# Performance work log

Measured on AMD Instinct MI355X. Metric: run time of the kernel, lower is better.

The kernel has to match this reference:

```python
import jax, jax.numpy as jnp
import numpy as np

N_CODEBOOKS = 4
CODEBOOK_SIZE = 1024
CODEBOOK_DIM = 8
INPUT_DIM = 512
EPS_NORM = 1e-12  # F.normalize eps
EPS_SCALE = 1e-8


def _normalize(x, eps=EPS_NORM):
    n = jnp.linalg.norm(x, axis=-1, keepdims=True)
    return x / jnp.maximum(n, eps)


def _wn_weight(v, g):
    # weight-norm 1x1 conv weight: v [out, in], g [out]
    return g[:, None] * v / jnp.maximum(jnp.linalg.norm(v, axis=1, keepdims=True), EPS_NORM)


def _vq_step(residual, v_in, g_in, b_in, v_out, g_out, b_out, cb):
    # residual: [B, D, T]
    sg = jax.lax.stop_gradient
    w_in = _wn_weight(v_in, g_in)                                   # [cd, D]
    z_e = jnp.einsum('od,bdt->bot', w_in, residual) + b_in[None, :, None]  # [B, cd, T]

    # nearest-code search on L2-normalized vectors (same argmin as the cdist form)
    enc = jnp.transpose(z_e, (0, 2, 1))                             # [B, T, cd]
    sim = jnp.einsum('btd,kd->btk', _normalize(enc), _normalize(cb))
    idx = jnp.argmax(sim, axis=-1)                                  # [B, T]
    q_tok = cb[idx]                                                 # [B, T, cd]
    z_q_pre = jnp.transpose(q_tok, (0, 2, 1))                       # [B, cd, T]

    commit = jnp.mean((z_e - sg(z_q_pre)) ** 2, axis=(1, 2))        # [B]
    codeb = jnp.mean((z_q_pre - sg(z_e)) ** 2, axis=(1, 2))         # [B]

    # rotation trick: z_q = scale * (I - 2 r r^T + 2 q_n e_n^T) z_e, R/scale stop-grad
    e = enc                                                         # [B, T, cd]
    e_n = sg(_normalize(e))
    q_n = sg(_normalize(q_tok))
    r = sg(_normalize(e_n + q_n))
    scale = sg(jnp.linalg.norm(q_tok, axis=-1, keepdims=True)
               / jnp.maximum(jnp.linalg.norm(e, axis=-1, keepdims=True), EPS_SCALE))
    re = jnp.sum(r * e, axis=-1, keepdims=True)
    ene = jnp.sum(e_n * e, axis=-1, keepdims=True)
    z_rot = scale * (e - 2.0 * r * re + 2.0 * q_n * ene)            # [B, T, cd]
    z_q = jnp.transpose(z_rot, (0, 2, 1))                           # [B, cd, T]

    w_out = _wn_weight(v_out, g_out)                                # [D, cd]
    z_q_i = jnp.einsum('od,bdt->bot', w_out, z_q) + b_out[None, :, None]  # [B, D, T]
    return z_q_i, commit, codeb, idx


def setup_inputs() -> dict:
    key = jax.random.key(0)
    ks = jax.random.split(key, 8)
    B, D, T = 16, INPUT_DIM, 4096
    nq, K, cd = N_CODEBOOKS, CODEBOOK_SIZE, CODEBOOK_DIM
    return {
        'z': jax.random.normal(ks[0], (B, D, T), dtype=jnp.float32),
        'in_proj_v': jax.random.normal(ks[1], (nq, cd, D), dtype=jnp.float32) * (1.0 / np.sqrt(D)),
        'in_proj_g': jnp.ones((nq, cd), dtype=jnp.float32),
        'in_proj_b': jnp.zeros((nq, cd), dtype=jnp.float32),
        'out_proj_v': jax.random.normal(ks[2], (nq, D, cd), dtype=jnp.float32) * (1.0 / np.sqrt(cd)),
        'out_proj_g': jnp.ones((nq, D), dtype=jnp.float32),
        'out_proj_b': jnp.zeros((nq, D), dtype=jnp.float32),
        'codebooks': jax.random.normal(ks[3], (nq, K, cd), dtype=jnp.float32),
    }


def reference(z, in_proj_v, in_proj_g, in_proj_b, out_proj_v, out_proj_g, out_proj_b, codebooks):
    # eval-mode RVQ forward: all N_CODEBOOKS codebooks active (mask all ones)
    z_q = jnp.zeros_like(z)
    residual = z
    commitment_loss = jnp.float32(0.0)
    codebook_loss = jnp.float32(0.0)
    codes = []
    for i in range(N_CODEBOOKS):
        z_q_i, commit_i, codeb_i, idx_i = _vq_step(
            residual, in_proj_v[i], in_proj_g[i], in_proj_b[i],
            out_proj_v[i], out_proj_g[i], out_proj_b[i], codebooks[i])
        z_q = z_q + z_q_i
        residual = residual - z_q_i
        commitment_loss = commitment_loss + jnp.mean(commit_i)
        codebook_loss = codebook_loss + jnp.mean(codeb_i)
        codes.append(idx_i)
    return z_q, jnp.stack(codes, axis=0), commitment_loss, codebook_loss
```

## Files before the change

### kernel.cpp

```cpp
#include <hip/hip_runtime.h>
#include <cstddef>

#define NQ 4
#define KCODES 1024
#define CD 8
#define DIM 512
#define BATCH 16
#define TLEN 4096
#define TT 32
#define NTHREADS 512

#define WS_WIN  0
#define WS_WOUT (NQ * DIM * CD)
#define WS_CBN  (2 * NQ * DIM * CD)
#define OUT_ZQ 0
#define OUT_CODES ((size_t)BATCH * DIM * TLEN)
#define OUT_LOSS (OUT_CODES + (size_t)NQ * BATCH * TLEN)

__global__ void rvq_zero(float* out) {
  out[OUT_LOSS] = 0.f;
  out[OUT_LOSS + 1] = 0.f;
}

__global__ void rvq_prep(const float* __restrict__ inv, const float* __restrict__ ing,
                         const float* __restrict__ outv, const float* __restrict__ outg,
                         const float* __restrict__ cb, float* __restrict__ ws) {
  const int blk = blockIdx.x, tid = threadIdx.x;
  if (blk < 32) {
    const int i = blk >> 3, o = blk & 7;
    const float* v = inv + (size_t)(i * CD + o) * DIM;
    const float a = v[tid], b = v[tid + 256];
    float s = a * a + b * b;
    #pragma unroll
    for (int off = 32; off >= 1; off >>= 1) s += __shfl_xor(s, off);
    __shared__ float red[4];
    if ((tid & 63) == 0) red[tid >> 6] = s;
    __syncthreads();
    const float nrm = fmaxf(sqrtf(red[0] + red[1] + red[2] + red[3]), 1e-12f);
    const float g = ing[i * CD + o];
    ws[WS_WIN + (size_t)((i * DIM + tid) * CD) + o] = (g * a) / nrm;
    ws[WS_WIN + (size_t)((i * DIM + tid + 256) * CD) + o] = (g * b) / nrm;
  } else {
    const int rid = (blk - 32) * 256 + tid;
    if (rid < NQ * DIM) {
      const float* v = outv + (size_t)rid * CD;
      float vv[8]; float n2 = 0.f;
      #pragma unroll
      for (int o = 0; o < 8; ++o) { vv[o] = v[o]; n2 += vv[o] * vv[o]; }
      const float nrm = fmaxf(sqrtf(n2), 1e-12f);
      const float g = outg[rid];
      #pragma unroll
      for (int o = 0; o < 8; ++o) ws[WS_WOUT + (size_t)rid * CD + o] = (g * vv[o]) / nrm;
    } else {
      const int k = rid - NQ * DIM;
      const float* v = cb + (size_t)k * CD;
      float vv[8]; float n2 = 0.f;
      #pragma unroll
      for (int o = 0; o < 8; ++o) { vv[o] = v[o]; n2 += vv[o] * vv[o]; }
      const float nrm = fmaxf(sqrtf(n2), 1e-12f);
      #pragma unroll
      for (int o = 0; o < 8; ++o) ws[WS_CBN + (size_t)k * CD + o] = vv[o] / nrm;
    }
  }
}

__launch_bounds__(NTHREADS, 4)
__global__ void rvq_main(const float* __restrict__ z,
                         const float* __restrict__ b_in, const float* __restrict__ b_out,
                         const float* __restrict__ cb, const float* __restrict__ ws,
                         float* __restrict__ out) {
  extern __shared__ float lds[];
  float* res  = lds;
  float* part = lds + DIM * TT;
  float* ze   = part + 8 * TT * 9;
  float* sc   = ze + TT * 9;
  int*   idl  = (int*)(sc + 16 * TT);

  const int tid = threadIdx.x;
  const int bb = blockIdx.x >> 7;
  const int t0 = (blockIdx.x & 127) * TT;

  const float* zb = z + (size_t)bb * DIM * TLEN + t0;

  {
    const int q = tid & 7, d0 = tid >> 3;
    #pragma unroll
    for (int p = 0; p < 8; ++p) {
      const int d = d0 + p * 64;
      const float4 v = *(const float4*)(zb + (size_t)d * TLEN + q * 4);
      *(float4*)(res + d * TT + q * 4) = v;
    }
  }
  __syncthreads();

  const int t  = tid & 31;
  const int dc = tid >> 5;
  const int w  = tid >> 6;
  float loss_acc = 0.f;

  for (int i = 0; i < NQ; ++i) {
    float acc[8] = {0,0,0,0,0,0,0,0};
    {
      const float* wp = ws + WS_WIN + (size_t)(i * DIM + dc * 32) * CD;
      const float* rp = res + dc * 32 * TT + t;
      #pragma unroll 4
      for (int j = 0; j < 32; ++j) {
        const float r = rp[j * TT];
        const float4 w0 = *(const float4*)(wp + j * 8);
        const float4 w1 = *(const float4*)(wp + j * 8 + 4);
        acc[0] += w0.x * r; acc[1] += w0.y * r; acc[2] += w0.z * r; acc[3] += w0.w * r;
        acc[4] += w1.x * r; acc[5] += w1.y * r; acc[6] += w1.z * r; acc[7] += w1.w * r;
      }
    }
    #pragma unroll
    for (int o = 0; o < 8; ++o) acc[o] += __shfl_xor(acc[o], 32);
    if ((tid & 63) < 32) {
      float* pp = part + (w * TT + t) * 9;
      #pragma unroll
      for (int o = 0; o < 8; ++o) pp[o] = acc[o];
    }
    __syncthreads();
    if (tid < 256) {
      const int tt2 = tid >> 3, o = tid & 7;
      float s = b_in[i * CD + o];
      #pragma unroll
      for (int ww = 0; ww < 8; ++ww) s += part[(ww * TT + tt2) * 9 + o];
      ze[tt2 * 9 + o] = s;
    }
    __syncthreads();

    float e[8], en[8];
    #pragma unroll
    for (int o = 0; o < 8; ++o) e[o] = ze[t * 9 + o];
    float ne2 = 0.f;
    #pragma unroll
    for (int o = 0; o < 8; ++o) ne2 += e[o] * e[o];
    const float ne = sqrtf(ne2);
    const float ned = fmaxf(ne, 1e-12f);
    #pragma unroll
    for (int o = 0; o < 8; ++o) en[o] = e[o] / ned;

    float best = -1e30f; int bk = 0;
    {
      const float* cp = ws + WS_CBN + (size_t)(i * KCODES + dc * 64) * CD;
      #pragma unroll 4
      for (int k = 0; k < 64; ++k) {
        const float4 c0 = *(const float4*)(cp + k * 8);
        const float4 c1 = *(const float4*)(cp + k * 8 + 4);
        const float s = en[0]*c0.x + en[1]*c0.y + en[2]*c0.z + en[3]*c0.w
                      + en[4]*c1.x + en[5]*c1.y + en[6]*c1.z + en[7]*c1.w;
        if (s > best) { best = s; bk = dc * 64 + k; }
      }
    }
    sc[tid] = best;
    idl[tid] = bk;
    __syncthreads();
    best = -1e30f; bk = KCODES;
    #pragma unroll
    for (int cc = 0; cc < 16; ++cc) {
      const float s2 = sc[cc * TT + t];
      const int k2 = idl[cc * TT + t];
      if (s2 > best || (s2 == best && k2 < bk)) { best = s2; bk = k2; }
    }
    if (tid < TT) {
      out[OUT_CODES + (size_t)(i * BATCH + bb) * TLEN + t0 + tid] = (float)bk;
    }

    float qv[8];
    {
      const float* qp = cb + (size_t)(i * KCODES + bk) * CD;
      const float4 q0 = *(const float4*)qp;
      const float4 q1 = *(const float4*)(qp + 4);
      qv[0]=q0.x; qv[1]=q0.y; qv[2]=q0.z; qv[3]=q0.w;
      qv[4]=q1.x; qv[5]=q1.y; qv[6]=q1.z; qv[7]=q1.w;
    }
    if (tid < TT) {
      float s = 0.f;
      #pragma unroll
      for (int o = 0; o < 8; ++o) { const float d2 = e[o] - qv[o]; s += d2 * d2; }
      loss_acc += s;
    }
    float nq2 = 0.f;
    #pragma unroll
    for (int o = 0; o < 8; ++o) nq2 += qv[o] * qv[o];
    const float nq = sqrtf(nq2);
    const float nqd = fmaxf(nq, 1e-12f);
    float qn[8], ru[8];
    float nr2 = 0.f;
    #pragma unroll
    for (int o = 0; o < 8; ++o) { qn[o] = qv[o] / nqd; ru[o] = en[o] + qn[o]; nr2 += ru[o] * ru[o]; }
    const float nrd = fmaxf(sqrtf(nr2), 1e-12f);
    const float scale = nq / fmaxf(ne, 1e-8f);
    float re = 0.f, ene = 0.f;
    #pragma unroll
    for (int o = 0; o < 8; ++o) { ru[o] = ru[o] / nrd; re += ru[o] * e[o]; ene += en[o] * e[o]; }
    float zr[8];
    #pragma unroll
    for (int o = 0; o < 8; ++o) zr[o] = scale * (e[o] - 2.f * ru[o] * re + 2.f * qn[o] * ene);

    {
      const float* wp2 = ws + WS_WOUT + (size_t)(i * DIM + dc * 32) * CD;
      const float* bp2 = b_out + i * DIM + dc * 32;
      float* rp2 = res + dc * 32 * TT + t;
      #pragma unroll 4
      for (int j = 0; j < 32; ++j) {
        const float4 w0 = *(const float4*)(wp2 + j * 8);
        const float4 w1 = *(const float4*)(wp2 + j * 8 + 4);
        float v = bp2[j];
        v += w0.x*zr[0] + w0.y*zr[1] + w0.z*zr[2] + w0.w*zr[3]
           + w1.x*zr[4] + w1.y*zr[5] + w1.z*zr[6] + w1.w*zr[7];
        rp2[j * TT] -= v;
      }
    }
    __syncthreads();
  }

  {
    const int q = tid & 7, d0 = tid >> 3;
    float* ob = out + OUT_ZQ + (size_t)bb * DIM * TLEN + t0;
    #pragma unroll
    for (int p = 0; p < 8; ++p) {
      const int d = d0 + p * 64;
      const float4 v = *(const float4*)(zb + (size_t)d * TLEN + q * 4);
      const float4 r4 = *(const float4*)(res + d * TT + q * 4);
      float4 ov; ov.x = v.x - r4.x; ov.y = v.y - r4.y; ov.z = v.z - r4.z; ov.w = v.w - r4.w;
      *(float4*)(ob + (size_t)d * TLEN + q * 4) = ov;
    }
  }

  #pragma unroll
  for (int off = 32; off >= 1; off >>= 1) loss_acc += __shfl_xor(loss_acc, off);
  if (tid == 0) {
    const float lv = loss_acc * (1.f / ((float)CD * TLEN * BATCH));
    atomicAdd(out + OUT_LOSS, lv);
    atomicAdd(out + OUT_LOSS + 1, lv);
  }
}

extern "C" void kernel_launch(void* const* d_in, const int* in_sizes, int n_in,
                              void* d_out, int out_size, void* d_ws, size_t ws_size,
                              hipStream_t stream) {
  const float* z    = (const float*)d_in[0];
  const float* inv  = (const float*)d_in[1];
  const float* ing  = (const float*)d_in[2];
  const float* inb  = (const float*)d_in[3];
  const float* outv = (const float*)d_in[4];
  const float* outg = (const float*)d_in[5];
  const float* outb = (const float*)d_in[6];
  const float* cbp  = (const float*)d_in[7];
  float* out = (float*)d_out;
  float* ws  = (float*)d_ws;

  hipLaunchKernelGGL(rvq_zero, dim3(1), dim3(1), 0, stream, out);
  hipLaunchKernelGGL(rvq_prep, dim3(56), dim3(256), 0, stream,
                     inv, ing, outv, outg, cbp, ws);
  hipLaunchKernelGGL(rvq_main, dim3(BATCH * (TLEN / TT)), dim3(NTHREADS),
                     80000, stream, z, inb, outb, cbp, ws, out);
}
```

Before: 771.9 us.

## Halve token tile, pad LDS rows, and reduce argmax with wave shuffles

Halves the per-block token tile from 32 to 16 and switches to static, padded shared memory (row stride 17), which roughly halves LDS use per block and allows more blocks per CU. The cross-chunk reductions for the projection and the argmax now use wave shuffles, which removes one barrier and the separate z_e reduction stage. The nearest-code search scores unnormalized e, since dividing by a positive norm does not change the argmax, and the rotation math is rewritten with reciprocals. In exchange, the global z loads and stores become 64-byte segments per row instead of 128-byte, and the padding forces scalar LDS accesses instead of float4.

Result: slower. 818.0 us (+6.0%).

```diff
diff --git a/kernel.cpp b/kernel.cpp
--- a/kernel.cpp
+++ b/kernel.cpp
@@ -7,7 +7,8 @@
 #define DIM 512
 #define BATCH 16
 #define TLEN 4096
-#define TT 32
+#define TT 16
+#define RPAD 17
 #define NTHREADS 512
 
 #define WS_WIN  0
@@ -64,48 +65,46 @@
   }
 }
 
-__launch_bounds__(NTHREADS, 4)
+__launch_bounds__(NTHREADS, 8)
 __global__ void rvq_main(const float* __restrict__ z,
                          const float* __restrict__ b_in, const float* __restrict__ b_out,
                          const float* __restrict__ cb, const float* __restrict__ ws,
                          float* __restrict__ out) {
-  extern __shared__ float lds[];
-  float* res  = lds;
-  float* part = lds + DIM * TT;
-  float* ze   = part + 8 * TT * 9;
-  float* sc   = ze + TT * 9;
-  int*   idl  = (int*)(sc + 16 * TT);
+  __shared__ float res[DIM * RPAD];
+  __shared__ float part[8 * TT * 9];
+  __shared__ float sc[8 * TT];
+  __shared__ int   idl[8 * TT];
 
   const int tid = threadIdx.x;
-  const int bb = blockIdx.x >> 7;
-  const int t0 = (blockIdx.x & 127) * TT;
-
+  const int bb = blockIdx.x >> 8;
+  const int t0 = (blockIdx.x & 255) * TT;
   const float* zb = z + (size_t)bb * DIM * TLEN + t0;
 
   {
-    const int q = tid & 7, d0 = tid >> 3;
-    #pragma unroll
-    for (int p = 0; p < 8; ++p) {
-      const int d = d0 + p * 64;
+    const int q = tid & 3, d0 = tid >> 2;
+    #pragma unroll
+    for (int p = 0; p < 4; ++p) {
+      const int d = d0 + p * 128;
       const float4 v = *(const float4*)(zb + (size_t)d * TLEN + q * 4);
-      *(float4*)(res + d * TT + q * 4) = v;
+      float* rp = res + d * RPAD + q * 4;
+      rp[0] = v.x; rp[1] = v.y; rp[2] = v.z; rp[3] = v.w;
     }
   }
   __syncthreads();
 
-  const int t  = tid & 31;
-  const int dc = tid >> 5;
+  const int t  = tid & 15;
+  const int dc = tid >> 4;
   const int w  = tid >> 6;
   float loss_acc = 0.f;
 
   for (int i = 0; i < NQ; ++i) {
     float acc[8] = {0,0,0,0,0,0,0,0};
     {
-      const float* wp = ws + WS_WIN + (size_t)(i * DIM + dc * 32) * CD;
-      const float* rp = res + dc * 32 * TT + t;
-      #pragma unroll 4
-      for (int j = 0; j < 32; ++j) {
-        const float r = rp[j * TT];
+      const float* wp = ws + WS_WIN + (size_t)(i * DIM + dc * 16) * CD;
+      const float* rp = res + dc * 16 * RPAD + t;
+      #pragma unroll
+      for (int j = 0; j < 16; ++j) {
+        const float r = rp[j * RPAD];
         const float4 w0 = *(const float4*)(wp + j * 8);
         const float4 w1 = *(const float4*)(wp + j * 8 + 4);
         acc[0] += w0.x * r; acc[1] += w0.y * r; acc[2] += w0.z * r; acc[3] += w0.w * r;
@@ -113,53 +112,56 @@
       }
     }
     #pragma unroll
-    for (int o = 0; o < 8; ++o) acc[o] += __shfl_xor(acc[o], 32);
-    if ((tid & 63) < 32) {
+    for (int o = 0; o < 8; ++o) {
+      acc[o] += __shfl_xor(acc[o], 16);
+      acc[o] += __shfl_xor(acc[o], 32);
+    }
+    if ((tid & 63) < 16) {
       float* pp = part + (w * TT + t) * 9;
       #pragma unroll
       for (int o = 0; o < 8; ++o) pp[o] = acc[o];
     }
     __syncthreads();
-    if (tid < 256) {
-      const int tt2 = tid >> 3, o = tid & 7;
-      float s = b_in[i * CD + o];
-      #pragma unroll
-      for (int ww = 0; ww < 8; ++ww) s += part[(ww * TT + tt2) * 9 + o];
-      ze[tt2 * 9 + o] = s;
-    }
-    __syncthreads();
-
-    float e[8], en[8];
-    #pragma unroll
-    for (int o = 0; o < 8; ++o) e[o] = ze[t * 9 + o];
+
+    float e[8];
+    #pragma unroll
+    for (int o = 0; o < 8; ++o) e[o] = b_in[i * CD + o];
+    #pragma unroll
+    for (int w2 = 0; w2 < 8; ++w2) {
+      const float* pp = part + (w2 * TT + t) * 9;
+      #pragma unroll
+      for (int o = 0; o < 8; ++o) e[o] += pp[o];
+    }
     float ne2 = 0.f;
     #pragma unroll
     for (int o = 0; o < 8; ++o) ne2 += e[o] * e[o];
     const float ne = sqrtf(ne2);
-    const float ned = fmaxf(ne, 1e-12f);
-    #pragma unroll
-    for (int o = 0; o < 8; ++o) en[o] = e[o] / ned;
 
     float best = -1e30f; int bk = 0;
     {
-      const float* cp = ws + WS_CBN + (size_t)(i * KCODES + dc * 64) * CD;
+      const float* cp = ws + WS_CBN + (size_t)(i * KCODES + dc * 32) * CD;
       #pragma unroll 4
-      for (int k = 0; k < 64; ++k) {
+      for (int k = 0; k < 32; ++k) {
         const float4 c0 = *(const float4*)(cp + k * 8);
         const float4 c1 = *(const float4*)(cp + k * 8 + 4);
-        const float s = en[0]*c0.x + en[1]*c0.y + en[2]*c0.z + en[3]*c0.w
-                      + en[4]*c1.x + en[5]*c1.y + en[6]*c1.z + en[7]*c1.w;
-        if (s > best) { best = s; bk = dc * 64 + k; }
+        const float s = e[0]*c0.x + e[1]*c0.y + e[2]*c0.z + e[3]*c0.w
+                      + e[4]*c1.x + e[5]*c1.y + e[6]*c1.z + e[7]*c1.w;
+        if (s > best) { best = s; bk = dc * 32 + k; }
       }
     }
-    sc[tid] = best;
-    idl[tid] = bk;
+    #pragma unroll
+    for (int off = 16; off <= 32; off <<= 1) {
+      const float s2 = __shfl_xor(best, off);
+      const int   k2 = __shfl_xor(bk, off);
+      if (s2 > best || (s2 == best && k2 < bk)) { best = s2; bk = k2; }
+    }
+    if ((tid & 63) < 16) { sc[w * TT + t] = best; idl[w * TT + t] = bk; }
     __syncthreads();
     best = -1e30f; bk = KCODES;
     #pragma unroll
-    for (int cc = 0; cc < 16; ++cc) {
-      const float s2 = sc[cc * TT + t];
-      const int k2 = idl[cc * TT + t];
+    for (int w2 = 0; w2 < 8; ++w2) {
+      const float s2 = sc[w2 * TT + t];
+      const int   k2 = idl[w2 * TT + t];
       if (s2 > best || (s2 == best && k2 < bk)) { best = s2; bk = k2; }
     }
     if (tid < TT) {
@@ -174,62 +176,66 @@
       qv[0]=q0.x; qv[1]=q0.y; qv[2]=q0.z; qv[3]=q0.w;
       qv[4]=q1.x; qv[5]=q1.y; qv[6]=q1.z; qv[7]=q1.w;
     }
-    if (tid < TT) {
+    if (dc == 0) {
       float s = 0.f;
       #pragma unroll
       for (int o = 0; o < 8; ++o) { const float d2 = e[o] - qv[o]; s += d2 * d2; }
       loss_acc += s;
     }
+
+    const float rne = 1.f / fmaxf(ne, 1e-12f);
     float nq2 = 0.f;
     #pragma unroll
     for (int o = 0; o < 8; ++o) nq2 += qv[o] * qv[o];
     const float nq = sqrtf(nq2);
-    const float nqd = fmaxf(nq, 1e-12f);
-    float qn[8], ru[8];
-    float nr2 = 0.f;
-    #pragma unroll
-    for (int o = 0; o < 8; ++o) { qn[o] = qv[o] / nqd; ru[o] = en[o] + qn[o]; nr2 += ru[o] * ru[o]; }
-    const float nrd = fmaxf(sqrtf(nr2), 1e-12f);
+    const float rq = 1.f / fmaxf(nq, 1e-12f);
+    float ru[8]; float nr2 = 0.f;
+    #pragma unroll
+    for (int o = 0; o < 8; ++o) { ru[o] = e[o] * rne + qv[o] * rq; nr2 += ru[o] * ru[o]; }
+    const float rr = 1.f / fmaxf(sqrtf(nr2), 1e-12f);
     const float scale = nq / fmaxf(ne, 1e-8f);
-    float re = 0.f, ene = 0.f;
-    #pragma unroll
-    for (int o = 0; o < 8; ++o) { ru[o] = ru[o] / nrd; re += ru[o] * e[o]; ene += en[o] * e[o]; }
-    float zr[8];
-    #pragma unroll
-    for (int o = 0; o < 8; ++o) zr[o] = scale * (e[o] - 2.f * ru[o] * re + 2.f * qn[o] * ene);
-
-    {
-      const float* wp2 = ws + WS_WOUT + (size_t)(i * DIM + dc * 32) * CD;
-      const float* bp2 = b_out + i * DIM + dc * 32;
-      float* rp2 = res + dc * 32 * TT + t;
-      #pragma unroll 4
-      for (int j = 0; j < 32; ++j) {
+    float re = 0.f;
+    #pragma unroll
+    for (int o = 0; o < 8; ++o) { ru[o] *= rr; re += ru[o] * e[o]; }
+    const float ene = ne2 * rne;
+    #pragma unroll
+    for (int o = 0; o < 8; ++o)
+      e[o] = scale * (e[o] - 2.f * ru[o] * re + 2.f * (qv[o] * rq) * ene);
+
+    {
+      const float* wp2 = ws + WS_WOUT + (size_t)(i * DIM + dc * 16) * CD;
+      const float* bp2 = b_out + i * DIM + dc * 16;
+      float* rp2 = res + dc * 16 * RPAD + t;
+      #pragma unroll
+      for (int j = 0; j < 16; ++j) {
         const float4 w0 = *(const float4*)(wp2 + j * 8);
         const float4 w1 = *(const float4*)(wp2 + j * 8 + 4);
         float v = bp2[j];
-        v += w0.x*zr[0] + w0.y*zr[1] + w0.z*zr[2] + w0.w*zr[3]
-           + w1.x*zr[4] + w1.y*zr[5] + w1.z*zr[6] + w1.w*zr[7];
-        rp2[j * TT] -= v;
+        v += w0.x*e[0] + w0.y*e[1] + w0.z*e[2] + w0.w*e[3]
+           + w1.x*e[4] + w1.y*e[5] + w1.z*e[6] + w1.w*e[7];
+        rp2[j * RPAD] -= v;
       }
     }
     __syncthreads();
   }
 
   {
-    const int q = tid & 7, d0 = tid >> 3;
+    const int q = tid & 3, d0 = tid >> 2;
     float* ob = out + OUT_ZQ + (size_t)bb * DIM * TLEN + t0;
     #pragma unroll
-    for (int p = 0; p < 8; ++p) {
-      const int d = d0 + p * 64;
-      const float4 v = *(const float4*)(zb + (size_t)d * TLEN + q * 4);
-      const float4 r4 = *(const float4*)(res + d * TT + q * 4);
-      float4 ov; ov.x = v.x - r4.x; ov.y = v.y - r4.y; ov.z = v.z - r4.z; ov.w = v.w - r4.w;
-      *(float4*)(ob + (size_t)d * TLEN + q * 4) = ov;
-    }
-  }
-
-  #pragma unroll
-  for (int off = 32; off >= 1; off >>= 1) loss_acc += __shfl_xor(loss_acc, off);
+    for (int p = 0; p < 4; ++p) {
+      const int d = d0 + p * 128;
+      float4 v = *(const float4*)(zb + (size_t)d * TLEN + q * 4);
+      const float* rp = res + d * RPAD + q * 4;
+      v.x -= rp[0]; v.y -= rp[1]; v.z -= rp[2]; v.w -= rp[3];
+      *(float4*)(ob + (size_t)d * TLEN + q * 4) = v;
+    }
+  }
+
+  loss_acc += __shfl_xor(loss_acc, 8);
+  loss_acc += __shfl_xor(loss_acc, 4);
+  loss_acc += __shfl_xor(loss_acc, 2);
+  loss_acc += __shfl_xor(loss_acc, 1);
   if (tid == 0) {
     const float lv = loss_acc * (1.f / ((float)CD * TLEN * BATCH));
     atomicAdd(out + OUT_LOSS, lv);
@@ -255,5 +261,5 @@
   hipLaunchKernelGGL(rvq_prep, dim3(56), dim3(256), 0, stream,
                      inv, ing, outv, outg, cbp, ws);
   hipLaunchKernelGGL(rvq_main, dim3(BATCH * (TLEN / TT)), dim3(NTHREADS),
-                     80000, stream, z, inb, outb, cbp, ws, out);
-}
+                     0, stream, z, inb, outb, cbp, ws, out);
+}
```
